# Optimization experiments

Measured on AMD Instinct MI355X. Metric: run time of the kernel, lower is better.

## Reference

```python
import jax, jax.numpy as jnp
import numpy as np

NUM_USERS = 16384
NUM_ITEMS = 50000
EMBED_DIM = 64
BATCH = 16384
MAX_FRIENDS = 32


def setup_inputs() -> dict:
    key = jax.random.key(0)
    k = jax.random.split(key, 7)
    users = jax.random.randint(k[0], (BATCH,), 0, NUM_USERS, dtype=jnp.int64 if jax.config.jax_enable_x64 else jnp.int32)
    items = jax.random.randint(k[1], (BATCH,), 0, NUM_ITEMS, dtype=users.dtype)
    # padded ragged friend lists (social_dict): indices + valid counts (0 => user not in dict)
    friends = jax.random.randint(k[2], (NUM_USERS, MAX_FRIENDS), 0, NUM_USERS, dtype=users.dtype)
    friend_counts = jax.random.randint(k[3], (NUM_USERS,), 0, MAX_FRIENDS + 1, dtype=jnp.int32)
    user_emb = jax.random.normal(k[4], (NUM_USERS, EMBED_DIM), jnp.float32) * 0.05   # xavier-ish
    item_emb = jax.random.normal(k[5], (NUM_ITEMS, EMBED_DIM), jnp.float32) * 0.05
    user_friend = jax.random.uniform(k[6], (NUM_USERS, NUM_USERS), jnp.float32)      # nn.init.uniform_
    return {"users": users, "items": items, "friends": friends,
            "friend_counts": friend_counts, "user_emb": user_emb,
            "item_emb": item_emb, "user_friend": user_friend}


def reference(users, items, friends, friend_counts, user_emb, item_emb, user_friend):
    ue = user_emb[users]                    # [B, D]
    ie = item_emb[items]                    # [B, D]
    pos = jnp.sum(ue * ie, axis=-1)         # bmm(u, i) -> [B]

    # vectorized social_influence over the whole batch
    fr = friends[users]                     # [B, F] friend indices
    cnt = friend_counts[users]              # [B]
    fe = user_emb[fr]                       # [B, F, D] friend embeddings
    fi = jnp.einsum('bfd,bd->bf', fe, ie)   # friend_item_influ
    uf = user_friend[users[:, None], fr]    # [B, F] user_friend[user, friends]
    mask = (jnp.arange(MAX_FRIENDS)[None, :] < cnt[:, None]).astype(fi.dtype)
    denom = jnp.maximum(cnt, 1).astype(fi.dtype)
    influ = jnp.sum(fi * uf * mask, axis=-1) / denom   # 0 when cnt == 0 (user not in dict)
    return pos + influ
```

## Files before the change

kernel.cpp:

```cpp
#include <hip/hip_runtime.h>
#include <hip/hip_bf16.h>

#define NUM_USERS   16384
#define NUM_ITEMS   50000
#define EMBED_DIM   64
#define BATCH       16384
#define MAX_FRIENDS 32

__global__ __launch_bounds__(256) void bpr_kernel(
    const int* __restrict__ users,
    const int* __restrict__ items,
    const int* __restrict__ friends,
    const int* __restrict__ fcnt,
    const float* __restrict__ uemb,
    const float* __restrict__ iemb,
    const float* __restrict__ ufr,
    float* __restrict__ out)
{
    const int wave = threadIdx.x >> 6;
    const int lane = threadIdx.x & 63;
    const int b = blockIdx.x * 4 + wave;
    if (b >= BATCH) return;

    const int u  = users[b];
    const int it = items[b];

    const float ie = iemb[(size_t)it * EMBED_DIM + lane];
    const float ue = uemb[(size_t)u  * EMBED_DIM + lane];
    const int   cnt = fcnt[u];

    int   fid = 0;
    float w   = 0.0f;
    if (lane < MAX_FRIENDS) {
        fid = friends[(size_t)u * MAX_FRIENDS + lane];
        if (lane < cnt) {
            w = ufr[(size_t)u * NUM_USERS + fid];
        }
    }

    float acc = 0.0f;
    #pragma unroll
    for (int f = 0; f < MAX_FRIENDS; ++f) {
        const int   idx = __shfl(fid, f);
        const float wf  = __shfl(w,   f);
        acc = fmaf(wf, uemb[(size_t)idx * EMBED_DIM + lane], acc);
    }

    const float denom = (float)max(cnt, 1);
    float v = (ue + acc / denom) * ie;

    #pragma unroll
    for (int off = 32; off > 0; off >>= 1)
        v += __shfl_xor(v, off);

    if (lane == 0) out[b] = v;
}

extern "C" void kernel_launch(void* const* d_in, const int* in_sizes, int n_in,
                              void* d_out, int out_size, void* d_ws, size_t ws_size,
                              hipStream_t stream) {
    const int*   users   = (const int*)  d_in[0];
    const int*   items   = (const int*)  d_in[1];
    const int*   friends = (const int*)  d_in[2];
    const int*   fcnt    = (const int*)  d_in[3];
    const float* uemb    = (const float*)d_in[4];
    const float* iemb    = (const float*)d_in[5];
    const float* ufr     = (const float*)d_in[6];
    float*       out     = (float*)d_out;

    const int blocks = BATCH / 4;
    bpr_kernel<<<blocks, 256, 0, stream>>>(users, items, friends, fcnt,
                                           uemb, iemb, ufr, out);
}
```

Measured before the change: 21.48 us.

## Process two batch rows per wave with float4 loads and friend-split lanes

Each wave now handles two batch rows. Lanes are split into 4 groups of 16, and each group covers 8 friends using float4 embedding loads. Friend embedding loads are skipped for entries past the valid count, and the shuffles for friend ids and weights are removed. Both rows are reduced together, with the division by the friend count moved to the end by scaling the positive term. This raises memory-level parallelism and cuts gather instructions, at the cost of more registers per thread and half as many waves.

```diff
diff --git a/kernel.cpp b/kernel.cpp
--- a/kernel.cpp
+++ b/kernel.cpp
@@ -19,41 +19,77 @@
 {
     const int wave = threadIdx.x >> 6;
     const int lane = threadIdx.x & 63;
-    const int b = blockIdx.x * 4 + wave;
-    if (b >= BATCH) return;
+    const int wid  = blockIdx.x * 4 + wave;
+    const int b0 = wid * 2;
+    const int b1 = b0 + 1;
 
-    const int u  = users[b];
-    const int it = items[b];
+    const int g = lane >> 4;
+    const int q = lane & 15;
 
-    const float ie = iemb[(size_t)it * EMBED_DIM + lane];
-    const float ue = uemb[(size_t)u  * EMBED_DIM + lane];
-    const int   cnt = fcnt[u];
+    const int u0 = users[b0], u1 = users[b1];
+    const int i0 = items[b0], i1 = items[b1];
+    const int c0 = fcnt[u0],  c1 = fcnt[u1];
 
-    int   fid = 0;
-    float w   = 0.0f;
-    if (lane < MAX_FRIENDS) {
-        fid = friends[(size_t)u * MAX_FRIENDS + lane];
-        if (lane < cnt) {
-            w = ufr[(size_t)u * NUM_USERS + fid];
+    const float4 ieA = *(const float4*)(iemb + (size_t)i0 * EMBED_DIM + q * 4);
+    const float4 ieB = *(const float4*)(iemb + (size_t)i1 * EMBED_DIM + q * 4);
+    const float4 ueA = *(const float4*)(uemb + (size_t)u0 * EMBED_DIM + q * 4);
+    const float4 ueB = *(const float4*)(uemb + (size_t)u1 * EMBED_DIM + q * 4);
+
+    const int4 fA0 = *(const int4*)(friends + (size_t)u0 * MAX_FRIENDS + g * 8);
+    const int4 fA1 = *(const int4*)(friends + (size_t)u0 * MAX_FRIENDS + g * 8 + 4);
+    const int4 fB0 = *(const int4*)(friends + (size_t)u1 * MAX_FRIENDS + g * 8);
+    const int4 fB1 = *(const int4*)(friends + (size_t)u1 * MAX_FRIENDS + g * 8 + 4);
+    const int fidA[8] = { fA0.x, fA0.y, fA0.z, fA0.w, fA1.x, fA1.y, fA1.z, fA1.w };
+    const int fidB[8] = { fB0.x, fB0.y, fB0.z, fB0.w, fB1.x, fB1.y, fB1.z, fB1.w };
+
+    const float* urowA = ufr + (size_t)u0 * NUM_USERS;
+    const float* urowB = ufr + (size_t)u1 * NUM_USERS;
+
+    float4 accA = make_float4(0.f, 0.f, 0.f, 0.f);
+    float4 accB = make_float4(0.f, 0.f, 0.f, 0.f);
+    #pragma unroll
+    for (int i = 0; i < 8; ++i) {
+        const int src = g * 8 + i;
+        if (src < c0) {
+            const float wf = urowA[fidA[i]];
+            const float4 a = *(const float4*)(uemb + (size_t)fidA[i] * EMBED_DIM + q * 4);
+            accA.x = fmaf(wf, a.x, accA.x);
+            accA.y = fmaf(wf, a.y, accA.y);
+            accA.z = fmaf(wf, a.z, accA.z);
+            accA.w = fmaf(wf, a.w, accA.w);
+        }
+        if (src < c1) {
+            const float wf = urowB[fidB[i]];
+            const float4 a = *(const float4*)(uemb + (size_t)fidB[i] * EMBED_DIM + q * 4);
+            accB.x = fmaf(wf, a.x, accB.x);
+            accB.y = fmaf(wf, a.y, accB.y);
+            accB.z = fmaf(wf, a.z, accB.z);
+            accB.w = fmaf(wf, a.w, accB.w);
         }
     }
 
-    float acc = 0.0f;
-    #pragma unroll
-    for (int f = 0; f < MAX_FRIENDS; ++f) {
-        const int   idx = __shfl(fid, f);
-        const float wf  = __shfl(w,   f);
-        acc = fmaf(wf, uemb[(size_t)idx * EMBED_DIM + lane], acc);
+    float v0 = accA.x * ieA.x + accA.y * ieA.y + accA.z * ieA.z + accA.w * ieA.w;
+    float v1 = accB.x * ieB.x + accB.y * ieB.y + accB.z * ieB.z + accB.w * ieB.w;
+
+    const float d0 = (float)max(c0, 1);
+    const float d1 = (float)max(c1, 1);
+    if (g == 0) {
+        const float pA = ueA.x * ieA.x + ueA.y * ieA.y + ueA.z * ieA.z + ueA.w * ieA.w;
+        const float pB = ueB.x * ieB.x + ueB.y * ieB.y + ueB.z * ieB.z + ueB.w * ieB.w;
+        v0 = fmaf(d0, pA, v0);
+        v1 = fmaf(d1, pB, v1);
     }
 
-    const float denom = (float)max(cnt, 1);
-    float v = (ue + acc / denom) * ie;
+    #pragma unroll
+    for (int off = 32; off > 0; off >>= 1) {
+        v0 += __shfl_xor(v0, off);
+        v1 += __shfl_xor(v1, off);
+    }
 
-    #pragma unroll
-    for (int off = 32; off > 0; off >>= 1)
-        v += __shfl_xor(v, off);
-
-    if (lane == 0) out[b] = v;
+    if (lane == 0) {
+        out[b0] = v0 / d0;
+        out[b1] = v1 / d1;
+    }
 }
 
 extern "C" void kernel_launch(void* const* d_in, const int* in_sizes, int n_in,
@@ -68,7 +104,7 @@
     const float* ufr     = (const float*)d_in[6];
     float*       out     = (float*)d_out;
 
-    const int blocks = BATCH / 4;
+    const int blocks = BATCH / 8;
     bpr_kernel<<<blocks, 256, 0, stream>>>(users, items, friends, fcnt,
                                            uemb, iemb, ufr, out);
 }
```

Result: faster. 18.29 us (-14.9%).
